# Kernel optimization log

Hardware: AMD Instinct MI355X
Metric: run time of the kernel (lower is better)

## Reference

```python
import jax, jax.numpy as jnp
import numpy as np

H = 8       # heads
DH = 64     # dim_head
EPS = 1e-5  # LayerNorm eps (torch default)


def _ln(x, g, b):
    m = x.mean(-1, keepdims=True)
    v = x.var(-1, keepdims=True)
    return (x - m) / jnp.sqrt(v + EPS) * g + b


def setup_inputs() -> dict:
    key = jax.random.key(0)
    ks = jax.random.split(key, 8)
    B, N, D = 2, 2048, 512
    s = lambda k, shape: jax.random.normal(k, shape, jnp.float32) * 0.02
    return {
        "q": jax.random.normal(ks[0], (B, N, D), jnp.float32),
        "k": jax.random.normal(ks[1], (B, N, D), jnp.float32),
        "v": jax.random.normal(ks[2], (B, N, D), jnp.float32),
        "ln_g": jnp.ones((D,), jnp.float32),
        "ln_b": jnp.zeros((D,), jnp.float32),
        "W_in": s(ks[3], (H * DH, D)),          # Linear(dim, inner_dim, bias=False)
        "wp_w1": s(ks[4], (DH, 2 * DH)),         # Linear(2*dim_head, dim_head)
        "wp_b1": jnp.zeros((DH,), jnp.float32),
        "wp_ln_g": jnp.ones((DH,), jnp.float32),
        "wp_ln_b": jnp.zeros((DH,), jnp.float32),
        "wp_w2": s(ks[5], (1, DH)),              # Linear(dim_head, 1)
        "wp_b2": jnp.zeros((1,), jnp.float32),
        "W_out": s(ks[6], (D, H * DH)),          # Linear(inner_dim, dim)
        "b_out": jnp.zeros((D,), jnp.float32),
    }


def reference(q, k, v, ln_g, ln_b, W_in, wp_w1, wp_b1, wp_ln_g, wp_ln_b,
              wp_w2, wp_b2, W_out, b_out):
    B, N, D = q.shape

    def proj(t):
        x = _ln(t, ln_g, ln_b) @ W_in.T                 # [B, N, H*DH]
        return x.reshape(B, N, H, DH).transpose(2, 0, 1, 3)  # [H, B, N, DH]

    fq, fk, fv = proj(q), proj(k), proj(v)

    # cosine similarity component
    dots = jnp.einsum('hbnd,hbmd->hbnm', fq, fk)        # [H, B, N, N]
    qn = jnp.linalg.norm(fq, axis=-1)                   # [H, B, N]
    kn = jnp.linalg.norm(fk, axis=-1)
    cosine = dots / (qn[..., :, None] * kn[..., None, :])

    # mean-centered covariance component
    qc = fq - fq.mean(-1, keepdims=True)
    kc = fk - fk.mean(-1, keepdims=True)
    cov = jnp.einsum('hbnd,hbmd->hbnm', qc, kc) / DH    # [H, B, N, N]

    # dynamic per-head blend weight
    qg = fq.mean((1, 2))                                # [H, DH]
    kg = fk.mean((1, 2))
    feat = jnp.concatenate([qg, kg], axis=-1)           # [H, 2*DH]
    hid = jax.nn.relu(_ln(feat @ wp_w1.T + wp_b1, wp_ln_g, wp_ln_b))
    w = jax.nn.sigmoid(hid @ wp_w2.T + wp_b2)           # [H, 1]
    w = w.reshape(H, 1, 1, 1)

    blend = (1.0 - w) * cosine + w * cov                # no softmax in cosine variant
    out = jnp.einsum('hbnm,hbmd->hbnd', blend, fv)      # [H, B, N, DH]
    out = out.transpose(1, 2, 0, 3).reshape(B, N, H * DH)
    return out @ W_out.T + b_out
```

## Files before the change

kernel.cpp:

```cpp
#include <hip/hip_runtime.h>
#include <stdint.h>

#define CH 8
#define CDH 64
#define CB 2
#define CN 2048
#define CD 512

typedef float f32x4 __attribute__((ext_vector_type(4)));
typedef __bf16 bf16x8 __attribute__((ext_vector_type(8)));
typedef unsigned short u16;

#define MFMA(a, b, c) __builtin_amdgcn_mfma_f32_16x16x32_bf16((a), (b), (c), 0, 0, 0)
#define GLOAD16(g, l)                                                              \
  __builtin_amdgcn_global_load_lds((const __attribute__((address_space(1))) void*)(g), \
                                   (__attribute__((address_space(3))) void*)(l), 16, 0, 0)

__device__ __forceinline__ u16 f2bf(float f) {
  union { float f; unsigned u; } c; c.f = f;
  return (u16)((c.u + 0x7FFFu + ((c.u >> 16) & 1u)) >> 16);
}
__device__ __forceinline__ float bf2f(u16 h) {
  union { unsigned u; float f; } c; c.u = ((unsigned)h) << 16;
  return c.f;
}

__global__ __launch_bounds__(256) void ln_convw_kernel(const float* __restrict__ q,
                                                       const float* __restrict__ k,
                                                       const float* __restrict__ v,
                                                       const float* __restrict__ g,
                                                       const float* __restrict__ bb,
                                                       u16* __restrict__ xln,
                                                       const float* __restrict__ wi_f,
                                                       const float* __restrict__ wo_f,
                                                       u16* __restrict__ wi,
                                                       u16* __restrict__ wo) {
  int row = blockIdx.x;
  int tid = threadIdx.x;
  if (row >= 12288) {
    int i = (row - 12288) * 256 + tid;
    wi[i] = f2bf(wi_f[i]);
    wo[i] = f2bf(wo_f[i]);
    return;
  }
  int t = row >> 12;
  int rr = row & 4095;
  const float* src = (t == 0 ? q : (t == 1 ? k : v)) + (size_t)rr * CD;
  float x0 = src[tid], x1 = src[tid + 256];
  float s = x0 + x1, s2 = x0 * x0 + x1 * x1;
#pragma unroll
  for (int m = 1; m < 64; m <<= 1) { s += __shfl_xor(s, m); s2 += __shfl_xor(s2, m); }
  __shared__ float red[8];
  int w = tid >> 6;
  if ((tid & 63) == 0) { red[w] = s; red[4 + w] = s2; }
  __syncthreads();
  s = red[0] + red[1] + red[2] + red[3];
  s2 = red[4] + red[5] + red[6] + red[7];
  float mean = s * (1.f / 512.f);
  float var = s2 * (1.f / 512.f) - mean * mean;
  float rstd = rsqrtf(var + 1e-5f);
  u16* dst = xln + (size_t)row * CD;
  dst[tid]       = f2bf((x0 - mean) * rstd * g[tid] + bb[tid]);
  dst[tid + 256] = f2bf((x1 - mean) * rstd * g[tid + 256] + bb[tid + 256]);
}

template <int OUT_BF16, int ADD_BIAS, int DO_STATS>
__global__ __launch_bounds__(256) void gemm_bt(const u16* __restrict__ A,
                                               const u16* __restrict__ Bt,
                                               void* __restrict__ Cout,
                                               const float* __restrict__ bias,
                                               float* __restrict__ iqn,
                                               float* __restrict__ ikn,
                                               float* __restrict__ qgp,
                                               float* __restrict__ kgp) {
  __shared__ u16 Al[2][128 * 64];
  __shared__ u16 Bl[2][128 * 64];
  int tm = blockIdx.x * 128, tn = blockIdx.y * 128;
  int tid = threadIdx.x;
  int w = tid >> 6, l = tid & 63;
  int wr = w >> 1, wc = w & 1;
  int lo = l & 15, hi = l >> 4;

  f32x4 zz = {0.f, 0.f, 0.f, 0.f};
  f32x4 acc[4][4];
#pragma unroll
  for (int mi = 0; mi < 4; mi++)
#pragma unroll
    for (int ni = 0; ni < 4; ni++) acc[mi][ni] = zz;

  int rowA = 8 * w + (l >> 3);
  int sl = l & 7;

#pragma unroll
  for (int i = 0; i < 4; i++) {
    int rl = rowA + 32 * i;
    int sp = sl ^ (rl & 7);
    GLOAD16(A + (size_t)(tm + rl) * CD + sp * 8, (char*)Al[0] + w * 1024 + i * 4096);
    GLOAD16(Bt + (size_t)(tn + rl) * CD + sp * 8, (char*)Bl[0] + w * 1024 + i * 4096);
  }
  __syncthreads();

  int cur = 0;
  for (int kt = 0; kt < 8; ++kt) {
    if (kt + 1 < 8) {
      int nxt = cur ^ 1;
#pragma unroll
      for (int i = 0; i < 4; i++) {
        int rl = rowA + 32 * i;
        int sp = sl ^ (rl & 7);
        GLOAD16(A + (size_t)(tm + rl) * CD + (kt + 1) * 64 + sp * 8,
                (char*)Al[nxt] + w * 1024 + i * 4096);
        GLOAD16(Bt + (size_t)(tn + rl) * CD + (kt + 1) * 64 + sp * 8,
                (char*)Bl[nxt] + w * 1024 + i * 4096);
      }
    }
    const u16* Ac = Al[cur];
    const u16* Bc = Bl[cur];
#pragma unroll
    for (int kk = 0; kk < 2; kk++) {
      bf16x8 af[4], bfr[4];
#pragma unroll
      for (int mi = 0; mi < 4; mi++) {
        int row = wr * 64 + mi * 16 + lo;
        int slot = (hi + 4 * kk) ^ (row & 7);
        af[mi] = *(const bf16x8*)&Ac[row * 64 + slot * 8];
      }
#pragma unroll
      for (int ni = 0; ni < 4; ni++) {
        int row = wc * 64 + ni * 16 + lo;
        int slot = (hi + 4 * kk) ^ (row & 7);
        bfr[ni] = *(const bf16x8*)&Bc[row * 64 + slot * 8];
      }
#pragma unroll
      for (int mi = 0; mi < 4; mi++)
#pragma unroll
        for (int ni = 0; ni < 4; ni++)
          acc[mi][ni] = MFMA(af[mi], bfr[ni], acc[mi][ni]);
    }
    if (kt + 1 < 8) {
      __syncthreads();
      cur ^= 1;
    }
  }

  if (DO_STATS) {
    int tblk = blockIdx.x;
    bool isq = tblk < 32, isk = (tblk >= 32) && (tblk < 64);
    if (isq || isk) {
      int h = blockIdx.y * 2 + wc;
#pragma unroll
      for (int mi = 0; mi < 4; mi++)
#pragma unroll
        for (int rg = 0; rg < 4; rg++) {
          float s2 = 0.f;
#pragma unroll
          for (int ni = 0; ni < 4; ni++) {
            float vv = acc[mi][ni][rg];
            s2 += vv * vv;
          }
#pragma unroll
          for (int m = 1; m < 16; m <<= 1) s2 += __shfl_xor(s2, m);
          if (lo == 0) {
            int rowg = tm + wr * 64 + mi * 16 + hi * 4 + rg;
            int rloc = rowg & 4095;
            int b = rloc >> 11, n = rloc & 2047;
            size_t o = ((size_t)h * 2 + b) * CN + n;
            float inv = rsqrtf(s2);
            if (isq) iqn[o] = inv; else ikn[o] = inv;
          }
        }
      float cs[4];
#pragma unroll
      for (int ni = 0; ni < 4; ni++) {
        float s = 0.f;
#pragma unroll
        for (int mi = 0; mi < 4; mi++)
#pragma unroll
          for (int rg = 0; rg < 4; rg++) s += acc[mi][ni][rg];
        s += __shfl_xor(s, 16);
        s += __shfl_xor(s, 32);
        cs[ni] = s;
      }
      __syncthreads();
      float* redl = (float*)&Al[0][0];
      if (hi == 0)
#pragma unroll
        for (int ni = 0; ni < 4; ni++) redl[((wr * 2 + wc) * 4 + ni) * 16 + lo] = cs[ni];
      __syncthreads();
      if (wr == 0 && hi == 0) {
#pragma unroll
        for (int ni = 0; ni < 4; ni++) {
          float vsum = redl[((0 * 2 + wc) * 4 + ni) * 16 + lo] +
                       redl[((1 * 2 + wc) * 4 + ni) * 16 + lo];
          int col = ni * 16 + lo;
          float* dstp = isq ? qgp : kgp;
          dstp[((tblk & 31) * 8 + h) * 64 + col] = vsum;
        }
      }
    }
  }

#pragma unroll
  for (int mi = 0; mi < 4; mi++)
#pragma unroll
    for (int ni = 0; ni < 4; ni++) {
      int col = tn + wc * 64 + ni * 16 + lo;
      float bv = ADD_BIAS ? bias[col] : 0.f;
#pragma unroll
      for (int rg = 0; rg < 4; rg++) {
        int rowg = tm + wr * 64 + mi * 16 + hi * 4 + rg;
        float vout = acc[mi][ni][rg] + bv;
        if (OUT_BF16)
          ((u16*)Cout)[(size_t)rowg * CD + col] = f2bf(vout);
        else
          ((float*)Cout)[(size_t)rowg * CD + col] = vout;
      }
    }
}

__global__ __launch_bounds__(256) void transpose_kv(const u16* __restrict__ F1,
                                                    const u16* __restrict__ F2,
                                                    const float* __restrict__ ikn,
                                                    u16* __restrict__ fkT,
                                                    u16* __restrict__ fvT,
                                                    u16* __restrict__ fvhT) {
  int bid = blockIdx.x;
  int nt = bid & 31, b = (bid >> 5) & 1, h = bid >> 6;
  int hb = h * 2 + b;
  __shared__ u16 Tk[64 * 72];
  __shared__ u16 Tv[64 * 72];
  int tid = threadIdx.x;
  int n = tid >> 2;
#pragma unroll
  for (int p = 0; p < 2; p++) {
    int c = (tid & 3) + 4 * p;
    size_t src = ((size_t)(b * CN + nt * 64 + n) * CD) + h * 64 + c * 8;
    *(bf16x8*)&Tk[n * 72 + c * 8] = *(const bf16x8*)&F1[src];
    *(bf16x8*)&Tv[n * 72 + c * 8] = *(const bf16x8*)&F2[src];
  }
  __syncthreads();
  int d = tid >> 2;
  const float* ikn_hb = ikn + (size_t)hb * CN + nt * 64;
#pragma unroll
  for (int p = 0; p < 2; p++) {
    int c = (tid & 3) + 4 * p;
    u16 tk[8], tv[8], th[8];
#pragma unroll
    for (int j = 0; j < 8; j++) {
      tk[j] = Tk[(c * 8 + j) * 72 + d];
      tv[j] = Tv[(c * 8 + j) * 72 + d];
      th[j] = f2bf(bf2f(tv[j]) * ikn_hb[c * 8 + j]);
    }
    size_t dst = (((size_t)hb * 64 + d) * CN) + nt * 64 + c * 8;
    *(bf16x8*)&fkT[dst] = *(bf16x8*)tk;
    *(bf16x8*)&fvT[dst] = *(bf16x8*)tv;
    *(bf16x8*)&fvhT[dst] = *(bf16x8*)th;
  }
}

__global__ __launch_bounds__(256) void gemm_M(const u16* __restrict__ fkT,
                                              const u16* __restrict__ fvT,
                                              const u16* __restrict__ fvhT,
                                              float* __restrict__ Mpart) {
  int bid = blockIdx.x;
  int hb = bid & 15, ms = bid >> 4;
  int tid = threadIdx.x, w = tid >> 6, l = tid & 63;
  int lo = l & 15, hi = l >> 4;

  __shared__ u16 Ak[2][64 * 64];
  __shared__ u16 Bv[2][64 * 64];
  __shared__ u16 Bh[2][64 * 64];

  const u16* Ab = fkT + (size_t)hb * 64 * CN;
  const u16* Vb = fvT + (size_t)hb * 64 * CN;
  const u16* Hb = fvhT + (size_t)hb * 64 * CN;

  f32x4 zz = {0.f, 0.f, 0.f, 0.f};
  f32x4 acc[2][4];
#pragma unroll
  for (int mat = 0; mat < 2; mat++)
#pragma unroll
    for (int dt = 0; dt < 4; dt++) acc[mat][dt] = zz;

  int rls = 8 * w + (l >> 3);
  int sls = l & 7;

  auto STAGE = [&](int kt, int slot) {
    int mc = ms * 512 + kt * 64;
#pragma unroll
    for (int i = 0; i < 2; i++) {
      int row = rls + 32 * i;
      int sp = sls ^ (row & 7);
      GLOAD16(Ab + (size_t)row * CN + mc + sp * 8, (char*)Ak[slot] + w * 1024 + i * 4096);
      GLOAD16(Vb + (size_t)row * CN + mc + sp * 8, (char*)Bv[slot] + w * 1024 + i * 4096);
      GLOAD16(Hb + (size_t)row * CN + mc + sp * 8, (char*)Bh[slot] + w * 1024 + i * 4096);
    }
  };

  STAGE(0, 0);
  __syncthreads();

  int cur = 0;
  for (int kt = 0; kt < 8; ++kt) {
    if (kt + 1 < 8) STAGE(kt + 1, cur ^ 1);
#pragma unroll
    for (int kk = 0; kk < 2; kk++) {
      int arow = w * 16 + lo;
      int aslot = (hi + 4 * kk) ^ (arow & 7);
      bf16x8 af = *(const bf16x8*)&Ak[cur][arow * 64 + aslot * 8];
#pragma unroll
      for (int dt = 0; dt < 4; dt++) {
        int brow = dt * 16 + lo;
        int bslot = (hi + 4 * kk) ^ (brow & 7);
        bf16x8 bh = *(const bf16x8*)&Bh[cur][brow * 64 + bslot * 8];
        bf16x8 bv = *(const bf16x8*)&Bv[cur][brow * 64 + bslot * 8];
        acc[0][dt] = MFMA(af, bh, acc[0][dt]);
        acc[1][dt] = MFMA(af, bv, acc[1][dt]);
      }
    }
    if (kt + 1 < 8) {
      __syncthreads();
      cur ^= 1;
    }
  }

  float* outp = Mpart + ((size_t)(hb * 4 + ms)) * 8192;
#pragma unroll
  for (int mat = 0; mat < 2; mat++)
#pragma unroll
    for (int dt = 0; dt < 4; dt++) {
      int d = dt * 16 + lo;
#pragma unroll
      for (int rg = 0; rg < 4; rg++) {
        int j = mat * 64 + w * 16 + hi * 4 + rg;
        outp[j * 64 + d] = acc[mat][dt][rg];
      }
    }
}

__global__ __launch_bounds__(256) void reduceM_mlp(const float* __restrict__ Mpart,
                                                   const float* __restrict__ qgp,
                                                   const float* __restrict__ kgp,
                                                   const float* __restrict__ w1,
                                                   const float* __restrict__ b1,
                                                   const float* __restrict__ lng,
                                                   const float* __restrict__ lnb,
                                                   const float* __restrict__ w2,
                                                   const float* __restrict__ b2,
                                                   u16* __restrict__ Bmat) {
  int hb = blockIdx.x;
  int h = hb >> 1;
  int tid = threadIdx.x;
  __shared__ float qg[64], kg[64], abg[3];
  if (tid < 64) {
    float s1 = 0.f, s2 = 0.f;
#pragma unroll
    for (int c = 0; c < 32; c++) {
      s1 += qgp[(c * 8 + h) * 64 + tid];
      s2 += kgp[(c * 8 + h) * 64 + tid];
    }
    qg[tid] = s1 * (1.f / 4096.f);
    kg[tid] = s2 * (1.f / 4096.f);
  }
  __syncthreads();
  if (tid < 64) {
    float acc = b1[tid];
#pragma unroll 8
    for (int i = 0; i < 64; i++)
      acc += qg[i] * w1[tid * 128 + i] + kg[i] * w1[tid * 128 + 64 + i];
    float s1 = acc, s2 = acc * acc;
#pragma unroll
    for (int m = 1; m < 64; m <<= 1) { s1 += __shfl_xor(s1, m); s2 += __shfl_xor(s2, m); }
    float mean = s1 * (1.f / 64.f);
    float var = s2 * (1.f / 64.f) - mean * mean;
    float y = (acc - mean) * rsqrtf(var + 1e-5f) * lng[tid] + lnb[tid];
    float hid = fmaxf(y, 0.f);
    float t = hid * w2[tid];
#pragma unroll
    for (int m = 1; m < 64; m <<= 1) t += __shfl_xor(t, m);
    float wv = 1.f / (1.f + expf(-(t + b2[0])));
    if (tid == 0) { abg[0] = 1.f - wv; abg[1] = wv * (1.f / 64.f); abg[2] = wv; }
  }
  __syncthreads();
  float alpha = abg[0], beta = abg[1], gamma = abg[2];

  __shared__ float Ms[128 * 65];
  __shared__ float S2s[64];
#pragma unroll
  for (int e = 0; e < 32; e++) {
    int idx = e * 256 + tid;
    int j = idx >> 6, d = idx & 63;
    float s = 0.f;
#pragma unroll
    for (int ms = 0; ms < 4; ms++)
      s += Mpart[((size_t)(hb * 4 + ms)) * 8192 + idx];
    Ms[j * 65 + d] = s;
  }
  __syncthreads();
  if (tid < 64) {
    float s = 0.f;
#pragma unroll
    for (int i = 0; i < 64; i++) s += Ms[(64 + i) * 65 + tid];
    S2s[tid] = s;
  }
  __syncthreads();
#pragma unroll
  for (int e = 0; e < 32; e++) {
    int idx = e * 256 + tid;
    int jr = idx >> 6, ic = idx & 63;
    float v;
    if (jr < 64) v = alpha * Ms[ic * 65 + jr];
    else {
      int d = jr - 64;
      v = beta * Ms[(64 + ic) * 65 + d] - (gamma * (1.f / 4096.f)) * S2s[d];
    }
    Bmat[(size_t)hb * 8192 + idx] = f2bf(v);
  }
}

__global__ __launch_bounds__(256) void gemm_out(const u16* __restrict__ F0,
                                                const u16* __restrict__ Bmat,
                                                const float* __restrict__ iqn,
                                                u16* __restrict__ A2) {
  int bid = blockIdx.x;
  int hb = bid >> 4, qt = bid & 15;
  int b = hb & 1, h = hb >> 1;
  int tid = threadIdx.x, w = tid >> 6, l = tid & 63;
  int lo = l & 15, hi = l >> 4;
  int qbase = qt * 128;

  const u16* Bm = Bmat + (size_t)hb * 8192;
  bf16x8 bm[8][2];
#pragma unroll
  for (int jt = 0; jt < 8; jt++)
#pragma unroll
    for (int kk = 0; kk < 2; kk++)
      bm[jt][kk] = *(const bf16x8*)&Bm[(jt * 16 + lo) * 64 + hi * 8 + kk * 32];

  f32x4 zz = {0.f, 0.f, 0.f, 0.f};
  f32x4 acc[2][8];
#pragma unroll
  for (int f = 0; f < 2; f++)
#pragma unroll
    for (int jt = 0; jt < 8; jt++) acc[f][jt] = zz;

#pragma unroll
  for (int f = 0; f < 2; f++) {
    const u16* qp = F0 + ((size_t)(b * CN + qbase + w * 32 + f * 16 + lo)) * CD +
                    h * 64 + hi * 8;
    bf16x8 a0 = *(const bf16x8*)qp;
    bf16x8 a1 = *(const bf16x8*)(qp + 32);
#pragma unroll
    for (int jt = 0; jt < 8; jt++) {
      acc[f][jt] = MFMA(a0, bm[jt][0], acc[f][jt]);
      acc[f][jt] = MFMA(a1, bm[jt][1], acc[f][jt]);
    }
  }

  const float* iqn_hb = iqn + (size_t)hb * CN;
#pragma unroll
  for (int f = 0; f < 2; f++) {
    float iqv[4];
    int nb = qbase + w * 32 + f * 16 + hi * 4;
#pragma unroll
    for (int rg = 0; rg < 4; rg++) iqv[rg] = iqn_hb[nb + rg];
#pragma unroll
    for (int jt = 0; jt < 4; jt++) {
      int d = jt * 16 + lo;
#pragma unroll
      for (int rg = 0; rg < 4; rg++) {
        float vout = iqv[rg] * acc[f][jt][rg] + acc[f][jt + 4][rg];
        int n = nb + rg;
        A2[((size_t)(b * CN + n)) * CD + h * 64 + d] = f2bf(vout);
      }
    }
  }
}

extern "C" void kernel_launch(void* const* d_in, const int* in_sizes, int n_in,
                              void* d_out, int out_size, void* d_ws, size_t ws_size,
                              hipStream_t stream) {
  const float* q = (const float*)d_in[0];
  const float* k = (const float*)d_in[1];
  const float* v = (const float*)d_in[2];
  const float* ln_g = (const float*)d_in[3];
  const float* ln_b = (const float*)d_in[4];
  const float* W_in = (const float*)d_in[5];
  const float* wp_w1 = (const float*)d_in[6];
  const float* wp_b1 = (const float*)d_in[7];
  const float* wp_lng = (const float*)d_in[8];
  const float* wp_lnb = (const float*)d_in[9];
  const float* wp_w2 = (const float*)d_in[10];
  const float* wp_b2 = (const float*)d_in[11];
  const float* W_out = (const float*)d_in[12];
  const float* b_out = (const float*)d_in[13];

  char* ws = (char*)d_ws;
  u16* xln = (u16*)(ws + 0);
  u16* F = (u16*)(ws + 12582912);
  u16* Wi = (u16*)(ws + 25165824);
  u16* Wo = (u16*)(ws + 25690112);
  u16* fkT = (u16*)(ws + 26214400);
  u16* fvT = (u16*)(ws + 30408704);
  u16* fvhT = (u16*)(ws + 34603008);
  u16* A2 = (u16*)(ws + 38797312);
  float* iqn = (float*)(ws + 42991616);
  float* ikn = (float*)(ws + 43122688);
  float* qgp = (float*)(ws + 43253760);
  float* kgp = (float*)(ws + 43319296);
  float* Mpart = (float*)(ws + 43384832);
  u16* Bmat = (u16*)(ws + 45481984);

  u16* F0 = F;
  u16* F1 = F + 2097152;
  u16* F2 = F + 4194304;

  ln_convw_kernel<<<13312, 256, 0, stream>>>(q, k, v, ln_g, ln_b, xln,
                                             W_in, W_out, Wi, Wo);
  gemm_bt<1, 0, 1><<<dim3(96, 4), 256, 0, stream>>>(xln, Wi, (void*)F, nullptr,
                                                    iqn, ikn, qgp, kgp);
  transpose_kv<<<512, 256, 0, stream>>>(F1, F2, ikn, fkT, fvT, fvhT);
  gemm_M<<<64, 256, 0, stream>>>(fkT, fvT, fvhT, Mpart);
  reduceM_mlp<<<16, 256, 0, stream>>>(Mpart, qgp, kgp, wp_w1, wp_b1,
                                      wp_lng, wp_lnb, wp_w2, wp_b2, Bmat);
  gemm_out<<<256, 256, 0, stream>>>(F0, Bmat, iqn, A2);
  gemm_bt<0, 1, 0><<<dim3(32, 4), 256, 0, stream>>>(A2, Wo, d_out, b_out,
                                                    nullptr, nullptr, nullptr, nullptr);
}
```

Baseline: 72.11 us.

## Fuse K/V transpose into projection GEMM epilogue and scale K on the fly

The projection GEMM epilogue now writes K and V tiles straight to their transposed per-head layout through LDS, so the row-major F1/F2 buffers are no longer stored. This removes the separate transpose_kv kernel and one launch. gemm_M no longer reads a precomputed fvhT buffer. It loads K into registers, multiplies by the inverse key norms, and writes a scaled copy into LDS, which cuts global traffic but adds VALU work and register pressure inside the main loop. The K/V GEMM blocks also do extra LDS transposes and syncs in the epilogue.

After: 61.54 us. -14.7%, faster.

```diff
diff --git a/kernel.cpp b/kernel.cpp
--- a/kernel.cpp
+++ b/kernel.cpp
@@ -10,6 +10,7 @@
 typedef float f32x4 __attribute__((ext_vector_type(4)));
 typedef __bf16 bf16x8 __attribute__((ext_vector_type(8)));
 typedef unsigned short u16;
+typedef unsigned int u32;
 
 #define MFMA(a, b, c) __builtin_amdgcn_mfma_f32_16x16x32_bf16((a), (b), (c), 0, 0, 0)
 #define GLOAD16(g, l)                                                              \
@@ -64,7 +65,7 @@
   dst[tid + 256] = f2bf((x1 - mean) * rstd * g[tid + 256] + bb[tid + 256]);
 }
 
-template <int OUT_BF16, int ADD_BIAS, int DO_STATS>
+template <int OUT_BF16, int ADD_BIAS, int MODE>
 __global__ __launch_bounds__(256) void gemm_bt(const u16* __restrict__ A,
                                                const u16* __restrict__ Bt,
                                                void* __restrict__ Cout,
@@ -72,9 +73,12 @@
                                                float* __restrict__ iqn,
                                                float* __restrict__ ikn,
                                                float* __restrict__ qgp,
-                                               float* __restrict__ kgp) {
-  __shared__ u16 Al[2][128 * 64];
-  __shared__ u16 Bl[2][128 * 64];
+                                               float* __restrict__ kgp,
+                                               u16* __restrict__ fkT,
+                                               u16* __restrict__ fvT) {
+  __shared__ u16 S[4][8192];
+#define AL_(s) (S[s])
+#define BL_(s) (S[2 + (s)])
   int tm = blockIdx.x * 128, tn = blockIdx.y * 128;
   int tid = threadIdx.x;
   int w = tid >> 6, l = tid & 63;
@@ -95,8 +99,8 @@
   for (int i = 0; i < 4; i++) {
     int rl = rowA + 32 * i;
     int sp = sl ^ (rl & 7);
-    GLOAD16(A + (size_t)(tm + rl) * CD + sp * 8, (char*)Al[0] + w * 1024 + i * 4096);
-    GLOAD16(Bt + (size_t)(tn + rl) * CD + sp * 8, (char*)Bl[0] + w * 1024 + i * 4096);
+    GLOAD16(A + (size_t)(tm + rl) * CD + sp * 8, (char*)AL_(0) + w * 1024 + i * 4096);
+    GLOAD16(Bt + (size_t)(tn + rl) * CD + sp * 8, (char*)BL_(0) + w * 1024 + i * 4096);
   }
   __syncthreads();
 
@@ -109,13 +113,13 @@
         int rl = rowA + 32 * i;
         int sp = sl ^ (rl & 7);
         GLOAD16(A + (size_t)(tm + rl) * CD + (kt + 1) * 64 + sp * 8,
-                (char*)Al[nxt] + w * 1024 + i * 4096);
+                (char*)AL_(nxt) + w * 1024 + i * 4096);
         GLOAD16(Bt + (size_t)(tn + rl) * CD + (kt + 1) * 64 + sp * 8,
-                (char*)Bl[nxt] + w * 1024 + i * 4096);
-      }
-    }
-    const u16* Ac = Al[cur];
-    const u16* Bc = Bl[cur];
+                (char*)BL_(nxt) + w * 1024 + i * 4096);
+      }
+    }
+    const u16* Ac = AL_(cur);
+    const u16* Bc = BL_(cur);
 #pragma unroll
     for (int kk = 0; kk < 2; kk++) {
       bf16x8 af[4], bfr[4];
@@ -143,11 +147,10 @@
     }
   }
 
-  if (DO_STATS) {
+  if (MODE == 1) {
     int tblk = blockIdx.x;
-    bool isq = tblk < 32, isk = (tblk >= 32) && (tblk < 64);
-    if (isq || isk) {
-      int h = blockIdx.y * 2 + wc;
+    int h = blockIdx.y * 2 + wc;
+    if (tblk < 32) {
 #pragma unroll
       for (int mi = 0; mi < 4; mi++)
 #pragma unroll
@@ -161,12 +164,9 @@
 #pragma unroll
           for (int m = 1; m < 16; m <<= 1) s2 += __shfl_xor(s2, m);
           if (lo == 0) {
-            int rowg = tm + wr * 64 + mi * 16 + hi * 4 + rg;
-            int rloc = rowg & 4095;
+            int rloc = tm + wr * 64 + mi * 16 + hi * 4 + rg;
             int b = rloc >> 11, n = rloc & 2047;
-            size_t o = ((size_t)h * 2 + b) * CN + n;
-            float inv = rsqrtf(s2);
-            if (isq) iqn[o] = inv; else ikn[o] = inv;
+            iqn[((size_t)h * 2 + b) * CN + n] = rsqrtf(s2);
           }
         }
       float cs[4];
@@ -182,7 +182,7 @@
         cs[ni] = s;
       }
       __syncthreads();
-      float* redl = (float*)&Al[0][0];
+      float* redl = (float*)&S[0][0];
       if (hi == 0)
 #pragma unroll
         for (int ni = 0; ni < 4; ni++) redl[((wr * 2 + wc) * 4 + ni) * 16 + lo] = cs[ni];
@@ -192,11 +192,92 @@
         for (int ni = 0; ni < 4; ni++) {
           float vsum = redl[((0 * 2 + wc) * 4 + ni) * 16 + lo] +
                        redl[((1 * 2 + wc) * 4 + ni) * 16 + lo];
-          int col = ni * 16 + lo;
-          float* dstp = isq ? qgp : kgp;
-          dstp[((tblk & 31) * 8 + h) * 64 + col] = vsum;
+          qgp[(tblk * 8 + h) * 64 + ni * 16 + lo] = vsum;
         }
       }
+    } else {
+      bool isk = tblk < 64;
+      u16* dstT = isk ? fkT : fvT;
+      int rloc0 = tm - (isk ? 4096 : 8192);
+      int bb2 = rloc0 >> 11, n0 = rloc0 & 2047;
+      float csk[4];
+      if (isk) {
+#pragma unroll
+        for (int mi = 0; mi < 4; mi++)
+#pragma unroll
+          for (int rg = 0; rg < 4; rg++) {
+            float s2 = 0.f;
+#pragma unroll
+            for (int ni = 0; ni < 4; ni++) {
+              float vv = acc[mi][ni][rg];
+              s2 += vv * vv;
+            }
+#pragma unroll
+            for (int m = 1; m < 16; m <<= 1) s2 += __shfl_xor(s2, m);
+            if (lo == 0) {
+              int n = n0 + wr * 64 + mi * 16 + hi * 4 + rg;
+              ikn[((size_t)h * 2 + bb2) * CN + n] = rsqrtf(s2);
+            }
+          }
+#pragma unroll
+        for (int ni = 0; ni < 4; ni++) {
+          float s = 0.f;
+#pragma unroll
+          for (int mi = 0; mi < 4; mi++)
+#pragma unroll
+            for (int rg = 0; rg < 4; rg++) s += acc[mi][ni][rg];
+          s += __shfl_xor(s, 16);
+          s += __shfl_xor(s, 32);
+          csk[ni] = s;
+        }
+      }
+      __syncthreads();
+      u16* Sf = &S[0][0];
+      int reg = wc * 2 + wr;
+#pragma unroll
+      for (int mi = 0; mi < 4; mi++)
+#pragma unroll
+        for (int ni = 0; ni < 4; ni++) {
+          int d = ni * 16 + lo;
+          int m0 = mi * 16 + hi * 4;
+          u16 t4[4];
+#pragma unroll
+          for (int rg = 0; rg < 4; rg++) t4[rg] = f2bf(acc[mi][ni][rg]);
+          int off = (reg * 64 + d) * 64 + (m0 ^ ((d & 7) << 3));
+          *(uint2*)&Sf[off] = *(const uint2*)t4;
+        }
+      __syncthreads();
+      {
+        int head = tid >> 7, c = tid & 127;
+        int hg = blockIdx.y * 2 + head;
+        size_t base = ((size_t)(hg * 2 + bb2)) * 64 * CN;
+#pragma unroll
+        for (int p = 0; p < 8; p++) {
+          int flat = p * 128 + c;
+          int d = flat >> 4, mc = flat & 15;
+          int wr2 = mc >> 3, m64 = (mc & 7) * 8;
+          int off = ((head * 2 + wr2) * 64 + d) * 64 + (m64 ^ ((d & 7) << 3));
+          bf16x8 vv = *(const bf16x8*)&Sf[off];
+          *(bf16x8*)&dstT[base + (size_t)d * CN + n0 + mc * 8] = vv;
+        }
+      }
+      if (isk) {
+        __syncthreads();
+        float* redl = (float*)&S[0][0];
+        if (hi == 0)
+#pragma unroll
+          for (int ni = 0; ni < 4; ni++) redl[((wr * 2 + wc) * 4 + ni) * 16 + lo] = csk[ni];
+        __syncthreads();
+        if (wr == 0 && hi == 0) {
+#pragma unroll
+          for (int ni = 0; ni < 4; ni++) {
+            float vsum = redl[((0 * 2 + wc) * 4 + ni) * 16 + lo] +
+                         redl[((1 * 2 + wc) * 4 + ni) * 16 + lo];
+            kgp[((tblk - 32) * 8 + h) * 64 + ni * 16 + lo] = vsum;
+          }
+        }
+      }
+      return;
     }
   }
 
@@ -216,64 +297,27 @@
           ((float*)Cout)[(size_t)rowg * CD + col] = vout;
       }
     }
-}
-
-__global__ __launch_bounds__(256) void transpose_kv(const u16* __restrict__ F1,
-                                                    const u16* __restrict__ F2,
-                                                    const float* __restrict__ ikn,
-                                                    u16* __restrict__ fkT,
-                                                    u16* __restrict__ fvT,
-                                                    u16* __restrict__ fvhT) {
-  int bid = blockIdx.x;
-  int nt = bid & 31, b = (bid >> 5) & 1, h = bid >> 6;
-  int hb = h * 2 + b;
-  __shared__ u16 Tk[64 * 72];
-  __shared__ u16 Tv[64 * 72];
-  int tid = threadIdx.x;
-  int n = tid >> 2;
-#pragma unroll
-  for (int p = 0; p < 2; p++) {
-    int c = (tid & 3) + 4 * p;
-    size_t src = ((size_t)(b * CN + nt * 64 + n) * CD) + h * 64 + c * 8;
-    *(bf16x8*)&Tk[n * 72 + c * 8] = *(const bf16x8*)&F1[src];
-    *(bf16x8*)&Tv[n * 72 + c * 8] = *(const bf16x8*)&F2[src];
-  }
-  __syncthreads();
-  int d = tid >> 2;
-  const float* ikn_hb = ikn + (size_t)hb * CN + nt * 64;
-#pragma unroll
-  for (int p = 0; p < 2; p++) {
-    int c = (tid & 3) + 4 * p;
-    u16 tk[8], tv[8], th[8];
-#pragma unroll
-    for (int j = 0; j < 8; j++) {
-      tk[j] = Tk[(c * 8 + j) * 72 + d];
-      tv[j] = Tv[(c * 8 + j) * 72 + d];
-      th[j] = f2bf(bf2f(tv[j]) * ikn_hb[c * 8 + j]);
-    }
-    size_t dst = (((size_t)hb * 64 + d) * CN) + nt * 64 + c * 8;
-    *(bf16x8*)&fkT[dst] = *(bf16x8*)tk;
-    *(bf16x8*)&fvT[dst] = *(bf16x8*)tv;
-    *(bf16x8*)&fvhT[dst] = *(bf16x8*)th;
-  }
+#undef AL_
+#undef BL_
 }
 
 __global__ __launch_bounds__(256) void gemm_M(const u16* __restrict__ fkT,
                                               const u16* __restrict__ fvT,
-                                              const u16* __restrict__ fvhT,
+                                              const float* __restrict__ ikn,
                                               float* __restrict__ Mpart) {
   int bid = blockIdx.x;
   int hb = bid & 15, ms = bid >> 4;
   int tid = threadIdx.x, w = tid >> 6, l = tid & 63;
   int lo = l & 15, hi = l >> 4;
 
-  __shared__ u16 Ak[2][64 * 64];
-  __shared__ u16 Bv[2][64 * 64];
-  __shared__ u16 Bh[2][64 * 64];
+  __shared__ u16 GM[6][4096];
+#define AK_(s) (GM[s])
+#define AKH_(s) (GM[2 + (s)])
+#define BV_(s) (GM[4 + (s)])
 
   const u16* Ab = fkT + (size_t)hb * 64 * CN;
   const u16* Vb = fvT + (size_t)hb * 64 * CN;
-  const u16* Hb = fvhT + (size_t)hb * 64 * CN;
+  const float* ikb = ikn + (size_t)hb * CN;
 
   f32x4 zz = {0.f, 0.f, 0.f, 0.f};
   f32x4 acc[2][4];
@@ -285,40 +329,70 @@
   int rls = 8 * w + (l >> 3);
   int sls = l & 7;
 
-  auto STAGE = [&](int kt, int slot) {
+  bf16x8 areg[2];
+  f32x4 ikreg[2][2];
+
+  auto STAGEGL = [&](int kt, int slot) {
     int mc = ms * 512 + kt * 64;
 #pragma unroll
     for (int i = 0; i < 2; i++) {
       int row = rls + 32 * i;
       int sp = sls ^ (row & 7);
-      GLOAD16(Ab + (size_t)row * CN + mc + sp * 8, (char*)Ak[slot] + w * 1024 + i * 4096);
-      GLOAD16(Vb + (size_t)row * CN + mc + sp * 8, (char*)Bv[slot] + w * 1024 + i * 4096);
-      GLOAD16(Hb + (size_t)row * CN + mc + sp * 8, (char*)Bh[slot] + w * 1024 + i * 4096);
+      GLOAD16(Ab + (size_t)row * CN + mc + sp * 8, (char*)AK_(slot) + w * 1024 + i * 4096);
+      GLOAD16(Vb + (size_t)row * CN + mc + sp * 8, (char*)BV_(slot) + w * 1024 + i * 4096);
     }
   };
-
-  STAGE(0, 0);
+  auto LOADA = [&](int kt) {
+    int mc = ms * 512 + kt * 64;
+#pragma unroll
+    for (int i = 0; i < 2; i++) {
+      int row = rls + 32 * i;
+      int sp = sls ^ (row & 7);
+      areg[i] = *(const bf16x8*)&Ab[(size_t)row * CN + mc + sp * 8];
+      ikreg[i][0] = *(const f32x4*)&ikb[mc + sp * 8];
+      ikreg[i][1] = *(const f32x4*)&ikb[mc + sp * 8 + 4];
+    }
+  };
+  auto WRITEA = [&](int slot) {
+#pragma unroll
+    for (int i = 0; i < 2; i++) {
+      u16 outp[8];
+#pragma unroll
+      for (int j = 0; j < 4; j++) outp[j] = f2bf((float)areg[i][j] * ikreg[i][0][j]);
+#pragma unroll
+      for (int j = 0; j < 4; j++) outp[4 + j] = f2bf((float)areg[i][4 + j] * ikreg[i][1][j]);
+      *(bf16x8*)((char*)AKH_(slot) + w * 1024 + i * 4096 + l * 16) = *(const bf16x8*)outp;
+    }
+  };
+
+  LOADA(0);
+  STAGEGL(0, 0);
+  WRITEA(0);
   __syncthreads();
 
   int cur = 0;
   for (int kt = 0; kt < 8; ++kt) {
-    if (kt + 1 < 8) STAGE(kt + 1, cur ^ 1);
+    if (kt + 1 < 8) {
+      LOADA(kt + 1);
+      STAGEGL(kt + 1, cur ^ 1);
+    }
 #pragma unroll
     for (int kk = 0; kk < 2; kk++) {
       int arow = w * 16 + lo;
       int aslot = (hi + 4 * kk) ^ (arow & 7);
-      bf16x8 af = *(const bf16x8*)&Ak[cur][arow * 64 + aslot * 8];
+      bf16x8 af = *(const bf16x8*)&AK_(cur)[arow * 64 + aslot * 8];
+      bf16x8 afh = *(const bf16x8*)&AKH_(cur)[arow * 64 + aslot * 8];
 #pragma unroll
       for (int dt = 0; dt < 4; dt++) {
         int brow = dt * 16 + lo;
         int bslot = (hi + 4 * kk) ^ (brow & 7);
-        bf16x8 bh = *(const bf16x8*)&Bh[cur][brow * 64 + bslot * 8];
-        bf16x8 bv = *(const bf16x8*)&Bv[cur][brow * 64 + bslot * 8];
-        acc[0][dt] = MFMA(af, bh, acc[0][dt]);
+        bf16x8 bv = *(const bf16x8*)&BV_(cur)[brow * 64 + bslot * 8];
+        acc[0][dt] = MFMA(afh, bv, acc[0][dt]);
         acc[1][dt] = MFMA(af, bv, acc[1][dt]);
       }
     }
     if (kt + 1 < 8) {
+      WRITEA(cur ^ 1);
       __syncthreads();
       cur ^= 1;
     }
@@ -336,6 +410,9 @@
         outp[j * 64 + d] = acc[mat][dt][rg];
       }
     }
+#undef AK_
+#undef AKH_
+#undef BV_
 }
 
 __global__ __launch_bounds__(256) void reduceM_mlp(const float* __restrict__ Mpart,
@@ -497,33 +574,28 @@
 
   char* ws = (char*)d_ws;
   u16* xln = (u16*)(ws + 0);
-  u16* F = (u16*)(ws + 12582912);
-  u16* Wi = (u16*)(ws + 25165824);
-  u16* Wo = (u16*)(ws + 25690112);
-  u16* fkT = (u16*)(ws + 26214400);
-  u16* fvT = (u16*)(ws + 30408704);
-  u16* fvhT = (u16*)(ws + 34603008);
-  u16* A2 = (u16*)(ws + 38797312);
-  float* iqn = (float*)(ws + 42991616);
-  float* ikn = (float*)(ws + 43122688);
-  float* qgp = (float*)(ws + 43253760);
-  float* kgp = (float*)(ws + 43319296);
-  float* Mpart = (float*)(ws + 43384832);
-  u16* Bmat = (u16*)(ws + 45481984);
-
-  u16* F0 = F;
-  u16* F1 = F + 2097152;
-  u16* F2 = F + 4194304;
+  u16* F0 = (u16*)(ws + 12582912);
+  u16* Wi = (u16*)(ws + 16777216);
+  u16* Wo = (u16*)(ws + 17301504);
+  u16* fkT = (u16*)(ws + 17825792);
+  u16* fvT = (u16*)(ws + 22020096);
+  u16* A2 = (u16*)(ws + 26214400);
+  float* iqn = (float*)(ws + 30408704);
+  float* ikn = (float*)(ws + 30539776);
+  float* qgp = (float*)(ws + 30670848);
+  float* kgp = (float*)(ws + 30736384);
+  float* Mpart = (float*)(ws + 30801920);
+  u16* Bmat = (u16*)(ws + 32899072);
 
   ln_convw_kernel<<<13312, 256, 0, stream>>>(q, k, v, ln_g, ln_b, xln,
                                              W_in, W_out, Wi, Wo);
-  gemm_bt<1, 0, 1><<<dim3(96, 4), 256, 0, stream>>>(xln, Wi, (void*)F, nullptr,
-                                                    iqn, ikn, qgp, kgp);
-  transpose_kv<<<512, 256, 0, stream>>>(F1, F2, ikn, fkT, fvT, fvhT);
-  gemm_M<<<64, 256, 0, stream>>>(fkT, fvT, fvhT, Mpart);
+  gemm_bt<1, 0, 1><<<dim3(96, 4), 256, 0, stream>>>(xln, Wi, (void*)F0, nullptr,
+                                                    iqn, ikn, qgp, kgp, fkT, fvT);
+  gemm_M<<<64, 256, 0, stream>>>(fkT, fvT, ikn, Mpart);
   reduceM_mlp<<<16, 256, 0, stream>>>(Mpart, qgp, kgp, wp_w1, wp_b1,
                                       wp_lng, wp_lnb, wp_w2, wp_b2, Bmat);
   gemm_out<<<256, 256, 0, stream>>>(F0, Bmat, iqn, A2);
   gemm_bt<0, 1, 0><<<dim3(32, 4), 256, 0, stream>>>(A2, Wo, d_out, b_out,
-                                                    nullptr, nullptr, nullptr, nullptr);
-}
+                                                    nullptr, nullptr, nullptr,
+                                                    nullptr, nullptr, nullptr);
+}
```
